# Kernel tuning notes

Hardware: AMD Instinct MI355X
Metric: run time of the kernel (lower is better)

The kernel has to match this reference:

```python
import jax, jax.numpy as jnp
import numpy as np

E, T, H, I = 8, 1024, 2048, 1408

def setup_inputs() -> dict:
    key = jax.random.key(0)
    k1, k2, k3, k4 = jax.random.split(key, 4)
    scale = 1.0 / np.sqrt(H)
    return {
        "x": jax.random.normal(k1, (E, T, H), dtype=jnp.float32),
        "gate_proj": jax.random.normal(k2, (E, H, I), dtype=jnp.float32) * scale,
        "up_proj": jax.random.normal(k3, (E, H, I), dtype=jnp.float32) * scale,
        "down_proj": jax.random.normal(k4, (E, I, H), dtype=jnp.float32) * (1.0 / np.sqrt(I)),
    }

def reference(x, gate_proj, up_proj, down_proj):
    # x: [E, T, H]; per-expert SwiGLU MLP via batched matmuls
    gate = jax.nn.silu(jnp.einsum('eth,ehi->eti', x, gate_proj))
    up = jnp.einsum('eth,ehi->eti', x, up_proj)
    return jnp.einsum('eti,eih->eth', gate * up, down_proj)
```

## Files before the change

kernel.cpp:

```cpp
#include <hip/hip_runtime.h>
#include <hip/hip_bf16.h>
#include <stdint.h>

#define NE 8
#define NT 1024
#define NH 2048
#define NI 1408
#define NI2 (2 * NI)

typedef __attribute__((ext_vector_type(8))) short          bf16x8;
typedef __attribute__((ext_vector_type(8))) unsigned short u16x8;
typedef __attribute__((ext_vector_type(4))) unsigned short u16x4;
typedef __attribute__((ext_vector_type(4))) float          f32x4;

__device__ __forceinline__ unsigned short f2bf(float f) {
  union { float f; uint32_t u; } v; v.f = f;
  uint32_t u = v.u;
  return (unsigned short)((u + 0x7FFFu + ((u >> 16) & 1u)) >> 16);
}

__device__ __forceinline__ void gload_lds16(const void* g, void* l) {
  __builtin_amdgcn_global_load_lds(
      (const __attribute__((address_space(1))) uint32_t*)g,
      (__attribute__((address_space(3))) uint32_t*)l, 16, 0, 0);
}

#define WAITV0() asm volatile("s_waitcnt vmcnt(0)" ::: "memory")
#define BAR() do { __builtin_amdgcn_sched_barrier(0); \
                   __builtin_amdgcn_s_barrier();      \
                   __builtin_amdgcn_sched_barrier(0); } while (0)

__global__ __launch_bounds__(256) void cvt_bf16(const float* __restrict__ src,
                                                unsigned short* __restrict__ dst,
                                                int n8) {
  int i = blockIdx.x * blockDim.x + threadIdx.x;
  const int stride = gridDim.x * blockDim.x;
  for (; i < n8; i += stride) {
    const float4 f0 = ((const float4*)src)[i * 2];
    const float4 f1 = ((const float4*)src)[i * 2 + 1];
    u16x8 o;
    o[0] = f2bf(f0.x); o[1] = f2bf(f0.y); o[2] = f2bf(f0.z); o[3] = f2bf(f0.w);
    o[4] = f2bf(f1.x); o[5] = f2bf(f1.y); o[6] = f2bf(f1.z); o[7] = f2bf(f1.w);
    ((u16x8*)dst)[i] = o;
  }
}

__global__ __launch_bounds__(256) void transpose_cvt(
    const float* __restrict__ src, unsigned short* __restrict__ dst,
    int R, int C, long estride, int ilv, int radd) {
  __shared__ float tile[64][65];
  const int e  = blockIdx.z;
  const int c0 = blockIdx.x * 64;
  const int r0 = blockIdx.y * 64;
  const float* s = src + (size_t)e * R * C;
  unsigned short* d = dst + (size_t)e * estride;
  const int tid = threadIdx.x;
  const int tr  = tid >> 4;
  const int tc  = (tid & 15) * 4;
  #pragma unroll
  for (int it = 0; it < 4; ++it) {
    const int r = it * 16 + tr;
    float4 v = *(const float4*)(s + (size_t)(r0 + r) * C + c0 + tc);
    tile[r][tc + 0] = v.x; tile[r][tc + 1] = v.y;
    tile[r][tc + 2] = v.z; tile[r][tc + 3] = v.w;
  }
  __syncthreads();
  #pragma unroll
  for (int it = 0; it < 4; ++it) {
    const int oc = it * 16 + tr;
    const int c  = c0 + oc;
    const int ro = ilv ? ((((c >> 4) << 5) | (c & 15)) | radd) : c;
    u16x4 o;
    o[0] = f2bf(tile[tc + 0][oc]);
    o[1] = f2bf(tile[tc + 1][oc]);
    o[2] = f2bf(tile[tc + 2][oc]);
    o[3] = f2bf(tile[tc + 3][oc]);
    *(u16x4*)(d + (size_t)ro * R + r0 + tc) = o;
  }
}

template <int NBY, int KDIM, int MODE>
__global__ __launch_bounds__(256, 2) void gemm_async(
    const unsigned short* __restrict__ Ag,
    const unsigned short* __restrict__ Bg,
    void* __restrict__ outp) {
  constexpr int KT    = KDIM / 64;
  constexpr int CHUNK = NBY * 8;

  __shared__ __align__(16) unsigned short As[2][128 * 64];
  __shared__ __align__(16) unsigned short Bs[2][128 * 64];

  const int flat = blockIdx.x;
  const int orig = (flat & 7) * CHUNK + (flat >> 3);
  const int e    = orig / CHUNK;
  const int r    = orig % CHUNK;
  const int by   = r >> 3;
  const int bx   = r & 7;

  const int bm  = bx * 128;
  const int bnn = by * 128;

  const int tid  = threadIdx.x;
  const int lane = tid & 63;
  const int w    = tid >> 6;
  const int wrm  = (w >> 1) * 64;
  const int wcn  = (w & 1) * 64;

  const unsigned short* Ae = Ag + (size_t)e * 1024 * KDIM;
  const unsigned short* Be = Bg + (size_t)e * (NBY * 128) * KDIM;

  const int l8 = lane >> 3;
  const int jx = (lane & 7) ^ l8;
  const unsigned short* aA = Ae + (size_t)(bm  + w * 32 + l8) * KDIM + jx * 8;
  const unsigned short* aB = Be + (size_t)(bnn + w * 32 + l8) * KDIM + jx * 8;

  f32x4 acc[4][4];
  #pragma unroll
  for (int i = 0; i < 4; ++i)
    #pragma unroll
    for (int j = 0; j < 4; ++j) acc[i][j] = f32x4{0.f, 0.f, 0.f, 0.f};

  const int aoff = (lane & 15) * 128 + ((((lane >> 4) << 4)) ^ ((lane & 7) << 4));

  auto STAGE = [&](unsigned short* Ad, unsigned short* Bd, int t) {
    const int kb = t * 64;
    #pragma unroll
    for (int q = 0; q < 4; ++q)
      gload_lds16(aA + (size_t)q * 8 * KDIM + kb, Ad + (w * 32 + q * 8) * 64);
    #pragma unroll
    for (int q = 0; q < 4; ++q)
      gload_lds16(aB + (size_t)q * 8 * KDIM + kb, Bd + (w * 32 + q * 8) * 64);
  };

  auto ITER = [&](int t, const unsigned short* Ac, const unsigned short* Bc,
                  unsigned short* An, unsigned short* Bn) {
    WAITV0();
    BAR();
    const char* Ab = (const char*)Ac + wrm * 128;
    const char* Bb = (const char*)Bc + wcn * 128;
    bf16x8 a[4][2], b[4][2];
    #pragma unroll
    for (int mi = 0; mi < 4; ++mi) {
      a[mi][0] = *(const bf16x8*)(Ab + mi * 2048 + aoff);
      a[mi][1] = *(const bf16x8*)(Ab + mi * 2048 + (aoff ^ 64));
    }
    #pragma unroll
    for (int nj = 0; nj < 4; ++nj) {
      b[nj][0] = *(const bf16x8*)(Bb + nj * 2048 + aoff);
      b[nj][1] = *(const bf16x8*)(Bb + nj * 2048 + (aoff ^ 64));
    }
    if (t + 1 < KT) STAGE(An, Bn, t + 1);
    #pragma unroll
    for (int kk = 0; kk < 2; ++kk)
      #pragma unroll
      for (int mi = 0; mi < 4; ++mi)
        #pragma unroll
        for (int nj = 0; nj < 4; ++nj)
          acc[mi][nj] = __builtin_amdgcn_mfma_f32_16x16x32_bf16(
              a[mi][kk], b[nj][kk], acc[mi][nj], 0, 0, 0);
  };

  STAGE(As[0], Bs[0], 0);

  #pragma unroll 1
  for (int t = 0; t < KT; t += 2) {
    ITER(t,     As[0], Bs[0], As[1], Bs[1]);
    ITER(t + 1, As[1], Bs[1], As[0], Bs[0]);
  }

  const int crow = (lane >> 4) * 4;
  const int ccol = lane & 15;
  if constexpr (MODE == 0) {
    float* oe = (float*)outp + (size_t)e * 1024 * (NBY * 128);
    #pragma unroll
    for (int mi = 0; mi < 4; ++mi)
      #pragma unroll
      for (int nj = 0; nj < 4; ++nj)
        #pragma unroll
        for (int j = 0; j < 4; ++j) {
          const int row = bm + wrm + mi * 16 + crow + j;
          const int col = bnn + wcn + nj * 16 + ccol;
          oe[(size_t)row * (NBY * 128) + col] = acc[mi][nj][j];
        }
  } else {
    unsigned short* he = (unsigned short*)outp + (size_t)e * 1024 * (NBY * 64);
    const int hcb = by * 64 + (wcn >> 1);
    #pragma unroll
    for (int mi = 0; mi < 4; ++mi)
      #pragma unroll
      for (int p = 0; p < 2; ++p)
        #pragma unroll
        for (int j = 0; j < 4; ++j) {
          const float g = acc[mi][2 * p][j];
          const float u = acc[mi][2 * p + 1][j];
          const float sv = g / (1.0f + __expf(-g)) * u;
          const int row = bm + wrm + mi * 16 + crow + j;
          const int col = hcb + p * 16 + ccol;
          he[(size_t)row * (NBY * 64) + col] = f2bf(sv);
        }
  }
}

extern "C" void kernel_launch(void* const* d_in, const int* in_sizes, int n_in,
                              void* d_out, int out_size, void* d_ws, size_t ws_size,
                              hipStream_t stream) {
  const float* x    = (const float*)d_in[0];
  const float* gate = (const float*)d_in[1];
  const float* up   = (const float*)d_in[2];
  const float* down = (const float*)d_in[3];
  float* out = (float*)d_out;

  unsigned short* x_bf = (unsigned short*)d_ws;
  unsigned short* wcat = x_bf + (size_t)NE * NT * NH;
  unsigned short* dT   = wcat + (size_t)NE * NI2 * NH;
  unsigned short* hb   = dT   + (size_t)NE * NH * NI;

  cvt_bf16<<<2048, 256, 0, stream>>>(x, x_bf, NE * NT * NH / 8);

  transpose_cvt<<<dim3(NI / 64, NH / 64, NE), 256, 0, stream>>>(
      gate, wcat, NH, NI, (long)NI2 * NH, 1, 0);
  transpose_cvt<<<dim3(NI / 64, NH / 64, NE), 256, 0, stream>>>(
      up, wcat, NH, NI, (long)NI2 * NH, 1, 16);
  transpose_cvt<<<dim3(NH / 64, NI / 64, NE), 256, 0, stream>>>(
      down, dT, NI, NH, (long)NH * NI, 0, 0);

  gemm_async<22, NH, 1><<<NE * 22 * 8, 256, 0, stream>>>(x_bf, wcat, hb);
  gemm_async<16, NI, 0><<<NE * 16 * 8, 256, 0, stream>>>(hb, dT, out);
}
```

Measured before the change: 286.9 us.

## Use 256x128 GEMM tiles with K-step 32 and new LDS swizzle

Switches both GEMMs from 128x128 tiles with a 64-wide K step to 256x128 tiles with a 32-wide K step. Each wave now computes a 128x64 sub-tile (8x4 MFMA accumulators), and the LDS layout, swizzle and grid mapping are rewritten to match. The larger M tile raises arithmetic intensity per B load and halves the block count, giving fewer, heavier blocks. In exchange it doubles accumulator registers, which may hurt occupancy under the two-blocks-per-CU bound, and the shorter K step means twice as many barriers per GEMM.

```diff
diff --git a/kernel.cpp b/kernel.cpp
--- a/kernel.cpp
+++ b/kernel.cpp
@@ -80,84 +80,79 @@
 }
 
 template <int NBY, int KDIM, int MODE>
-__global__ __launch_bounds__(256, 2) void gemm_async(
+__global__ __launch_bounds__(256, 2) void gemm_bal(
     const unsigned short* __restrict__ Ag,
     const unsigned short* __restrict__ Bg,
     void* __restrict__ outp) {
-  constexpr int KT    = KDIM / 64;
-  constexpr int CHUNK = NBY * 8;
-
-  __shared__ __align__(16) unsigned short As[2][128 * 64];
-  __shared__ __align__(16) unsigned short Bs[2][128 * 64];
+  constexpr int KT    = KDIM / 32;
+  constexpr int CHUNK = 4 * NBY;
+
+  __shared__ __align__(16) unsigned short As[2][256 * 32];
+  __shared__ __align__(16) unsigned short Bs[2][128 * 32];
 
   const int flat = blockIdx.x;
   const int orig = (flat & 7) * CHUNK + (flat >> 3);
   const int e    = orig / CHUNK;
   const int r    = orig % CHUNK;
-  const int by   = r >> 3;
-  const int bx   = r & 7;
-
-  const int bm  = bx * 128;
+  const int bx   = r & 3;
+  const int by   = r >> 2;
+
+  const int bm  = bx * 256;
   const int bnn = by * 128;
 
   const int tid  = threadIdx.x;
   const int lane = tid & 63;
   const int w    = tid >> 6;
-  const int wrm  = (w >> 1) * 64;
+  const int wrm  = (w >> 1) * 128;
   const int wcn  = (w & 1) * 64;
 
   const unsigned short* Ae = Ag + (size_t)e * 1024 * KDIM;
   const unsigned short* Be = Bg + (size_t)e * (NBY * 128) * KDIM;
 
-  const int l8 = lane >> 3;
-  const int jx = (lane & 7) ^ l8;
-  const unsigned short* aA = Ae + (size_t)(bm  + w * 32 + l8) * KDIM + jx * 8;
-  const unsigned short* aB = Be + (size_t)(bnn + w * 32 + l8) * KDIM + jx * 8;
-
-  f32x4 acc[4][4];
+  const int l16 = lane >> 2;
+  const int jx  = (lane & 3) ^ ((lane >> 3) & 3);
+  const unsigned short* aA = Ae + (size_t)(bm  + w * 64 + l16) * KDIM + jx * 8;
+  const unsigned short* aB = Be + (size_t)(bnn + w * 32 + l16) * KDIM + jx * 8;
+
+  f32x4 acc[8][4];
   #pragma unroll
-  for (int i = 0; i < 4; ++i)
+  for (int i = 0; i < 8; ++i)
     #pragma unroll
     for (int j = 0; j < 4; ++j) acc[i][j] = f32x4{0.f, 0.f, 0.f, 0.f};
 
-  const int aoff = (lane & 15) * 128 + ((((lane >> 4) << 4)) ^ ((lane & 7) << 4));
+  const int aoff = (lane & 15) * 64 +
+                   (((lane >> 4) ^ (((lane & 15) >> 1) & 3)) * 16);
 
   auto STAGE = [&](unsigned short* Ad, unsigned short* Bd, int t) {
-    const int kb = t * 64;
+    const int kb = t * 32;
     #pragma unroll
     for (int q = 0; q < 4; ++q)
-      gload_lds16(aA + (size_t)q * 8 * KDIM + kb, Ad + (w * 32 + q * 8) * 64);
-    #pragma unroll
-    for (int q = 0; q < 4; ++q)
-      gload_lds16(aB + (size_t)q * 8 * KDIM + kb, Bd + (w * 32 + q * 8) * 64);
+      gload_lds16(aA + (size_t)q * 16 * KDIM + kb, Ad + (w * 64 + q * 16) * 32);
+    #pragma unroll
+    for (int q = 0; q < 2; ++q)
+      gload_lds16(aB + (size_t)q * 16 * KDIM + kb, Bd + (w * 32 + q * 16) * 32);
   };
 
   auto ITER = [&](int t, const unsigned short* Ac, const unsigned short* Bc,
                   unsigned short* An, unsigned short* Bn) {
     WAITV0();
     BAR();
-    const char* Ab = (const char*)Ac + wrm * 128;
-    const char* Bb = (const char*)Bc + wcn * 128;
-    bf16x8 a[4][2], b[4][2];
-    #pragma unroll
-    for (int mi = 0; mi < 4; ++mi) {
-      a[mi][0] = *(const bf16x8*)(Ab + mi * 2048 + aoff);
-      a[mi][1] = *(const bf16x8*)(Ab + mi * 2048 + (aoff ^ 64));
-    }
-    #pragma unroll
-    for (int nj = 0; nj < 4; ++nj) {
-      b[nj][0] = *(const bf16x8*)(Bb + nj * 2048 + aoff);
-      b[nj][1] = *(const bf16x8*)(Bb + nj * 2048 + (aoff ^ 64));
-    }
+    const char* Ab = (const char*)Ac + wrm * 64;
+    const char* Bb = (const char*)Bc + wcn * 64;
+    bf16x8 a[8], b[4];
+    #pragma unroll
+    for (int mi = 0; mi < 8; ++mi)
+      a[mi] = *(const bf16x8*)(Ab + mi * 1024 + aoff);
+    #pragma unroll
+    for (int nj = 0; nj < 4; ++nj)
+      b[nj] = *(const bf16x8*)(Bb + nj * 1024 + aoff);
     if (t + 1 < KT) STAGE(An, Bn, t + 1);
     #pragma unroll
-    for (int kk = 0; kk < 2; ++kk)
+    for (int mi = 0; mi < 8; ++mi)
       #pragma unroll
-      for (int mi = 0; mi < 4; ++mi)
-        #pragma unroll
-        for (int nj = 0; nj < 4; ++nj)
-          acc[mi][nj] = __builtin_amdgcn_mfma_f32_16x16x32_bf16(
-              a[mi][kk], b[nj][kk], acc[mi][nj], 0, 0, 0);
+      for (int nj = 0; nj < 4; ++nj)
+        acc[mi][nj] = __builtin_amdgcn_mfma_f32_16x16x32_bf16(
+            a[mi], b[nj], acc[mi][nj], 0, 0, 0);
   };
 
   STAGE(As[0], Bs[0], 0);
@@ -173,7 +168,7 @@
   if constexpr (MODE == 0) {
     float* oe = (float*)outp + (size_t)e * 1024 * (NBY * 128);
     #pragma unroll
-    for (int mi = 0; mi < 4; ++mi)
+    for (int mi = 0; mi < 8; ++mi)
       #pragma unroll
       for (int nj = 0; nj < 4; ++nj)
         #pragma unroll
@@ -186,7 +181,7 @@
     unsigned short* he = (unsigned short*)outp + (size_t)e * 1024 * (NBY * 64);
     const int hcb = by * 64 + (wcn >> 1);
     #pragma unroll
-    for (int mi = 0; mi < 4; ++mi)
+    for (int mi = 0; mi < 8; ++mi)
       #pragma unroll
       for (int p = 0; p < 2; ++p)
         #pragma unroll
@@ -224,6 +219,6 @@
   transpose_cvt<<<dim3(NH / 64, NI / 64, NE), 256, 0, stream>>>(
       down, dT, NI, NH, (long)NH * NI, 0, 0);
 
-  gemm_async<22, NH, 1><<<NE * 22 * 8, 256, 0, stream>>>(x_bf, wcat, hb);
-  gemm_async<16, NI, 0><<<NE * 16 * 8, 256, 0, stream>>>(hb, dT, out);
-}
+  gemm_bal<22, NH, 1><<<NE * 4 * 22, 256, 0, stream>>>(x_bf, wcat, hb);
+  gemm_bal<16, NI, 0><<<NE * 4 * 16, 256, 0, stream>>>(hb, dT, out);
+}
```

Result: no change. 285.4 us (-0.5%).
